# Performance work log

Hardware: AMD Instinct MI355X
Metric: run time of the kernel (lower is better)

The kernel has to match this reference:

```python
import jax, jax.numpy as jnp
import numpy as np

B, S, HID, NH, MAX_TOKENS = 2, 2048, 2048, 16, 2048
HD = HID // NH

def rotate_half(x):
    x1, x2 = x[..., :x.shape[-1] // 2], x[..., x.shape[-1] // 2:]
    return jnp.concatenate((-x2, x1), axis=-1)

def rope_tables():
    inv_freq = 1.0 / (10000.0 ** (jnp.arange(0, HD, 2, dtype=jnp.float32) / HD))
    t = jnp.arange(MAX_TOKENS, dtype=jnp.float32)
    freqs = jnp.outer(t, inv_freq)                       # [T, HD/2]
    emb = jnp.concatenate((freqs, freqs), axis=-1)       # [T, HD]
    return jnp.cos(emb), jnp.sin(emb)

def setup_inputs() -> dict:
    key = jax.random.key(0)
    ks = jax.random.split(key, 5)
    hidden_states = jax.random.normal(ks[0], (B, S, HID), dtype=jnp.float32)
    # additive causal mask [B, 1, S, S]: 0 on/below diag, large negative above
    neg = jnp.finfo(jnp.float32).min
    causal = jnp.where(jnp.tril(jnp.ones((S, S), dtype=bool)), 0.0, neg)
    attention_mask = jnp.broadcast_to(causal[None, None], (B, 1, S, S)).astype(jnp.float32)
    position_ids = jnp.broadcast_to(jnp.arange(S, dtype=jnp.int32), (B, S))
    scale = 1.0 / np.sqrt(HID)
    Wq = jax.random.normal(ks[1], (HID, HID), dtype=jnp.float32) * scale
    Wk = jax.random.normal(ks[2], (HID, HID), dtype=jnp.float32) * scale
    Wv = jax.random.normal(ks[3], (HID, HID), dtype=jnp.float32) * scale
    Wo = jax.random.normal(ks[4], (HID, HID), dtype=jnp.float32) * scale
    return {"hidden_states": hidden_states, "attention_mask": attention_mask,
            "position_ids": position_ids, "Wq": Wq, "Wk": Wk, "Wv": Wv, "Wo": Wo}

def reference(hidden_states, attention_mask, position_ids, Wq, Wk, Wv, Wo):
    b, s, _ = hidden_states.shape
    def proj(W):  # torch Linear: x @ W.T -> [b, H, s, hd]
        return (hidden_states @ W.T).reshape(b, s, NH, HD).transpose(0, 2, 1, 3)
    q, k, v = proj(Wq), proj(Wk), proj(Wv)
    cos_t, sin_t = rope_tables()
    cos = cos_t[position_ids][:, None]   # [b, 1, s, hd]
    sin = sin_t[position_ids][:, None]
    q = q * cos + rotate_half(q) * sin
    k = k * cos + rotate_half(k) * sin
    scores = jnp.einsum('bhqd,bhkd->bhqk', q, k) / np.sqrt(HD)
    scores = jnp.maximum(scores + attention_mask, jnp.finfo(scores.dtype).min)
    attn = jax.nn.softmax(scores.astype(jnp.float32), axis=-1).astype(q.dtype)
    out = jnp.einsum('bhqk,bhkd->bhqd', attn, v)
    out = out.transpose(0, 2, 1, 3).reshape(b, s, HID)
    return out @ Wo.T
```

## Files before the change

### kernel.cpp

```cpp
#include <hip/hip_runtime.h>

#define B_   2
#define S_   2048
#define HID_ 2048
#define NH_  16
#define HD_  128
#define MAXTOK_ 2048

typedef float  f32x4  __attribute__((ext_vector_type(4)));
typedef __bf16 bf16x8 __attribute__((ext_vector_type(8)));
typedef unsigned short u16x8 __attribute__((ext_vector_type(8)));

__device__ __forceinline__ unsigned short f2bf(float f) {
  union { float fv; unsigned u; } v; v.fv = f;
  unsigned r = v.u + 0x7FFFu + ((v.u >> 16) & 1u);
  return (unsigned short)(r >> 16);
}
__device__ __forceinline__ float bf2f(unsigned short h) {
  union { unsigned u; float fv; } v; v.u = ((unsigned)h) << 16;
  return v.fv;
}

__device__ __forceinline__ void gload16(const void* g, void* lds) {
  __builtin_amdgcn_global_load_lds(
      (const __attribute__((address_space(1))) void*)g,
      (__attribute__((address_space(3))) void*)lds, 16, 0, 0);
}

#define H4_ (B_ * S_ * HID_ / 4)
#define W4_ (HID_ * HID_ / 4)
__global__ void cast_all(const float* __restrict__ h,  const float* __restrict__ wq,
                         const float* __restrict__ wk, const float* __restrict__ wv,
                         const float* __restrict__ wo,
                         unsigned short* __restrict__ xb,  unsigned short* __restrict__ wqb,
                         unsigned short* __restrict__ wkb, unsigned short* __restrict__ wvb,
                         unsigned short* __restrict__ wob) {
  const int total = H4_ + 4 * W4_;
  int i = blockIdx.x * blockDim.x + threadIdx.x;
  int stride = gridDim.x * blockDim.x;
  for (; i < total; i += stride) {
    const float* src; unsigned short* dst; int j;
    if (i < H4_) { src = h; dst = xb; j = i; }
    else {
      int k = i - H4_, wsel = k >> 20;
      j = k & (W4_ - 1);
      src = (wsel == 0) ? wq : (wsel == 1) ? wk : (wsel == 2) ? wv : wo;
      dst = (wsel == 0) ? wqb : (wsel == 1) ? wkb : (wsel == 2) ? wvb : wob;
    }
    float4 v = ((const float4*)src)[j];
    ushort4 o;
    o.x = f2bf(v.x); o.y = f2bf(v.y); o.z = f2bf(v.z); o.w = f2bf(v.w);
    ((ushort4*)dst)[j] = o;
  }
}

#define QKV_STG(gp, lp, rb) gload16((gp) + (size_t)(rb) * 2048, (lp) + (rb) * 64)

#define QKV_LOADA(Q) do { \
  _Pragma("unroll") \
  for (int mi_ = 0; mi_ < 2; ++mi_) { \
    const char* rp_ = (const char*)Acur + (size_t)((wm + (Q) * 32 + mi_ * 16 + rowq) * 128); \
    af[mi_][0] = *(const bf16x8*)(rp_ + cb0); \
    af[mi_][1] = *(const bf16x8*)(rp_ + cb1); \
  } } while (0)

#define QKV_LOADB() do { \
  _Pragma("unroll") \
  for (int ni_ = 0; ni_ < 3; ++ni_) { \
    const char* rp_ = (const char*)Bcur + (size_t)((wn + ni_ * 16 + rowq) * 128); \
    bfr[ni_][0] = *(const bf16x8*)(rp_ + cb0); \
    bfr[ni_][1] = *(const bf16x8*)(rp_ + cb1); \
  } } while (0)

#define QKV_MFMA(Q) do { \
  _Pragma("unroll") \
  for (int mi_ = 0; mi_ < 2; ++mi_) { \
    _Pragma("unroll") \
    for (int ni_ = 0; ni_ < 3; ++ni_) { \
      f32x4 c_ = acc[(Q) * 2 + mi_][ni_]; \
      c_ = __builtin_amdgcn_mfma_f32_16x16x32_bf16(af[mi_][0], bfr[ni_][0], c_, 0, 0, 0); \
      c_ = __builtin_amdgcn_mfma_f32_16x16x32_bf16(af[mi_][1], bfr[ni_][1], c_, 0, 0, 0); \
      acc[(Q) * 2 + mi_][ni_] = c_; \
    } } } while (0)

#define QKV_BAR    asm volatile("s_barrier" ::: "memory")
#define QKV_VMC4   asm volatile("s_waitcnt vmcnt(4)" ::: "memory")
#define QKV_VMC2   asm volatile("s_waitcnt vmcnt(2)" ::: "memory")
#define QKV_VMC0   asm volatile("s_waitcnt vmcnt(0)" ::: "memory")

__global__ __launch_bounds__(512, 2)
void gemm_qkv(const unsigned short* __restrict__ A,
              const unsigned short* __restrict__ Bw,
              unsigned short* __restrict__ Qb,
              unsigned short* __restrict__ Kb,
              unsigned short* __restrict__ Vtmp) {
  const int K = HID_;
  const int NT = K / 64;
  __shared__ __align__(16) unsigned short As[2][256 * 64];
  __shared__ __align__(16) unsigned short Bs[2][192 * 64];

  const int tid = threadIdx.x, lane = tid & 63, w = tid >> 6;
  const int n0 = blockIdx.x * 192, m0 = blockIdx.y * 256;
  const int wm = (w >> 2) * 128, wn = (w & 3) * 48;
  const int rowq = lane & 15, klane = lane >> 4;
  const int sw  = (rowq & 7) << 4;
  const int cb0 = (klane * 16) ^ sw;
  const int cb1 = ((klane + 4) * 16) ^ sw;
  const int srow = tid >> 3;
  const int dc8  = (tid & 7) * 8;
  const int scol = (((tid & 7) * 16) ^ ((srow & 7) << 4)) >> 1;

  const unsigned short* Ag = A  + (size_t)(m0 + srow) * K + scol;
  const unsigned short* Bg = Bw + (size_t)(n0 + srow) * K + scol;

  f32x4 acc[8][3];
#pragma unroll
  for (int i = 0; i < 8; ++i)
#pragma unroll
    for (int j = 0; j < 3; ++j)
#pragma unroll
      for (int r = 0; r < 4; ++r) acc[i][j][r] = 0.f;

  bf16x8 af[2][2], bfr[3][2];

  {
    unsigned short* Al = (unsigned short*)&As[0][0] + srow * 64 + dc8;
    unsigned short* Bl = (unsigned short*)&Bs[0][0] + srow * 64 + dc8;
    QKV_STG(Bg, Bl, 0); QKV_STG(Bg, Bl, 64); QKV_STG(Bg, Bl, 128);
    QKV_STG(Ag, Al, 0); QKV_STG(Ag, Al, 128);
    QKV_STG(Ag, Al, 64); QKV_STG(Ag, Al, 192);
  }
  QKV_VMC2;
  QKV_BAR;

  const unsigned short* Acur = &As[0][0];
  const unsigned short* Bcur = &Bs[0][0];
  unsigned short* Anx = (unsigned short*)&As[1][0];
  unsigned short* Bnx = (unsigned short*)&Bs[1][0];

  for (int t = 0; t < NT - 1; ++t) {
    const int kn = (t + 1) * 64;
    const unsigned short* Agk = Ag + kn;
    const unsigned short* Bgk = Bg + kn;
    unsigned short* Al = Anx + srow * 64 + dc8;
    unsigned short* Bl = Bnx + srow * 64 + dc8;

    QKV_LOADA(0); QKV_LOADB();
    QKV_STG(Bgk, Bl, 0); QKV_STG(Bgk, Bl, 64);
    QKV_BAR;
    __builtin_amdgcn_s_setprio(1); QKV_MFMA(0); __builtin_amdgcn_s_setprio(0);
    QKV_BAR;
    QKV_LOADA(1);
    QKV_STG(Bgk, Bl, 128); QKV_STG(Agk, Al, 0);
    QKV_BAR;
    __builtin_amdgcn_s_setprio(1); QKV_MFMA(1); __builtin_amdgcn_s_setprio(0);
    QKV_VMC4;
    QKV_BAR;
    QKV_LOADA(2);
    QKV_STG(Agk, Al, 128); QKV_STG(Agk, Al, 64);
    QKV_BAR;
    __builtin_amdgcn_s_setprio(1); QKV_MFMA(2); __builtin_amdgcn_s_setprio(0);
    QKV_BAR;
    QKV_LOADA(3);
    QKV_STG(Agk, Al, 192);
    QKV_BAR;
    __builtin_amdgcn_s_setprio(1); QKV_MFMA(3); __builtin_amdgcn_s_setprio(0);
    QKV_VMC2;
    QKV_BAR;

    { const unsigned short* tp = Acur; Acur = Anx; Anx = (unsigned short*)tp; }
    { const unsigned short* tp = Bcur; Bcur = Bnx; Bnx = (unsigned short*)tp; }
  }

  QKV_LOADA(0); QKV_LOADB();
  QKV_BAR;
  __builtin_amdgcn_s_setprio(1); QKV_MFMA(0); __builtin_amdgcn_s_setprio(0);
  QKV_BAR;
  QKV_LOADA(1);
  QKV_BAR;
  __builtin_amdgcn_s_setprio(1); QKV_MFMA(1); __builtin_amdgcn_s_setprio(0);
  QKV_VMC0;
  QKV_BAR;
  QKV_LOADA(2);
  QKV_BAR;
  __builtin_amdgcn_s_setprio(1); QKV_MFMA(2); __builtin_amdgcn_s_setprio(0);
  QKV_BAR;
  QKV_LOADA(3);
  __builtin_amdgcn_s_setprio(1); QKV_MFMA(3); __builtin_amdgcn_s_setprio(0);

  const int lr0 = klane * 4;
#pragma unroll
  for (int mi = 0; mi < 8; ++mi)
#pragma unroll
    for (int ni = 0; ni < 3; ++ni)
#pragma unroll
      for (int r = 0; r < 4; ++r) {
        int r_ = m0 + wm + mi * 16 + lr0 + r;
        int c_ = n0 + wn + ni * 16 + rowq;
        float v = acc[mi][ni][r];
        int b = r_ >> 11, s = r_ & 2047;
        int proj = c_ >> 11, cin = c_ & 2047;
        if (proj == 2) {
          Vtmp[(size_t)(b * S_ + s) * HID_ + cin] = f2bf(v);
        } else {
          int hh = cin >> 7, d = cin & 127;
          unsigned short* dst = (proj == 0) ? Qb : Kb;
          dst[(((size_t)(b * NH_ + hh) * S_ + s) * HD_) + d] = f2bf(v);
        }
      }
}

#define OUT_LOADB() do { \
  _Pragma("unroll") \
  for (int ni_ = 0; ni_ < 2; ++ni_) { \
    const char* rp_ = (const char*)Bcur + (size_t)((wn + ni_ * 16 + rowq) * 128); \
    bfr[ni_][0] = *(const bf16x8*)(rp_ + cb0); \
    bfr[ni_][1] = *(const bf16x8*)(rp_ + cb1); \
  } } while (0)

#define OUT_MFMA(Q) do { \
  _Pragma("unroll") \
  for (int mi_ = 0; mi_ < 2; ++mi_) { \
    _Pragma("unroll") \
    for (int ni_ = 0; ni_ < 2; ++ni_) { \
      f32x4 c_ = acc[(Q) * 2 + mi_][ni_]; \
      c_ = __builtin_amdgcn_mfma_f32_16x16x32_bf16(af[mi_][0], bfr[ni_][0], c_, 0, 0, 0); \
      c_ = __builtin_amdgcn_mfma_f32_16x16x32_bf16(af[mi_][1], bfr[ni_][1], c_, 0, 0, 0); \
      acc[(Q) * 2 + mi_][ni_] = c_; \
    } } } while (0)

__global__ __launch_bounds__(512, 2)
void gemm_out(const unsigned short* __restrict__ A,
              const unsigned short* __restrict__ Bw,
              float* __restrict__ Cout) {
  const int K = HID_, N = HID_;
  const int NT = K / 64;
  __shared__ __align__(16) unsigned short As[2][256 * 64];
  __shared__ __align__(16) unsigned short Bs[2][128 * 64];

  const int tid = threadIdx.x, lane = tid & 63, w = tid >> 6;
  const int n0 = blockIdx.x * 128, m0 = blockIdx.y * 256;
  const int wm = (w >> 2) * 128, wn = (w & 3) * 32;
  const int rowq = lane & 15, klane = lane >> 4;
  const int sw  = (rowq & 7) << 4;
  const int cb0 = (klane * 16) ^ sw;
  const int cb1 = ((klane + 4) * 16) ^ sw;
  const int srow = tid >> 3;
  const int dc8  = (tid & 7) * 8;
  const int scol = (((tid & 7) * 16) ^ ((srow & 7) << 4)) >> 1;

  const unsigned short* Ag = A  + (size_t)(m0 + srow) * K + scol;
  const unsigned short* Bg = Bw + (size_t)(n0 + srow) * K + scol;

  f32x4 acc[8][2];
#pragma unroll
  for (int i = 0; i < 8; ++i)
#pragma unroll
    for (int j = 0; j < 2; ++j)
#pragma unroll
      for (int r = 0; r < 4; ++r) acc[i][j][r] = 0.f;

  bf16x8 af[2][2], bfr[2][2];

  {
    unsigned short* Al = (unsigned short*)&As[0][0] + srow * 64 + dc8;
    unsigned short* Bl = (unsigned short*)&Bs[0][0] + srow * 64 + dc8;
    QKV_STG(Bg, Bl, 0); QKV_STG(Bg, Bl, 64);
    QKV_STG(Ag, Al, 0); QKV_STG(Ag, Al, 128);
    QKV_STG(Ag, Al, 64); QKV_STG(Ag, Al, 192);
  }
  QKV_VMC2;
  QKV_BAR;

  const unsigned short* Acur = &As[0][0];
  const unsigned short* Bcur = &Bs[0][0];
  unsigned short* Anx = (unsigned short*)&As[1][0];
  unsigned short* Bnx = (unsigned short*)&Bs[1][0];

  for (int t = 0; t < NT - 1; ++t) {
    const int kn = (t + 1) * 64;
    const unsigned short* Agk = Ag + kn;
    const unsigned short* Bgk = Bg + kn;
    unsigned short* Al = Anx + srow * 64 + dc8;
    unsigned short* Bl = Bnx + srow * 64 + dc8;

    QKV_LOADA(0); OUT_LOADB();
    QKV_STG(Bgk, Bl, 0); QKV_STG(Bgk, Bl, 64);
    QKV_BAR;
    __builtin_amdgcn_s_setprio(1); OUT_MFMA(0); __builtin_amdgcn_s_setprio(0);
    QKV_BAR;
    QKV_LOADA(1);
    QKV_STG(Agk, Al, 0); QKV_STG(Agk, Al, 128);
    QKV_BAR;
    __builtin_amdgcn_s_setprio(1); OUT_MFMA(1); __builtin_amdgcn_s_setprio(0);
    QKV_VMC4;
    QKV_BAR;
    QKV_LOADA(2);
    QKV_STG(Agk, Al, 64);
    QKV_BAR;
    __builtin_amdgcn_s_setprio(1); OUT_MFMA(2); __builtin_amdgcn_s_setprio(0);
    QKV_BAR;
    QKV_LOADA(3);
    QKV_STG(Agk, Al, 192);
    QKV_BAR;
    __builtin_amdgcn_s_setprio(1); OUT_MFMA(3); __builtin_amdgcn_s_setprio(0);
    QKV_VMC2;
    QKV_BAR;

    { const unsigned short* tp = Acur; Acur = Anx; Anx = (unsigned short*)tp; }
    { const unsigned short* tp = Bcur; Bcur = Bnx; Bnx = (unsigned short*)tp; }
  }

  QKV_LOADA(0); OUT_LOADB();
  QKV_BAR;
  __builtin_amdgcn_s_setprio(1); OUT_MFMA(0); __builtin_amdgcn_s_setprio(0);
  QKV_BAR;
  QKV_LOADA(1);
  QKV_BAR;
  __builtin_amdgcn_s_setprio(1); OUT_MFMA(1); __builtin_amdgcn_s_setprio(0);
  QKV_VMC0;
  QKV_BAR;
  QKV_LOADA(2);
  QKV_BAR;
  __builtin_amdgcn_s_setprio(1); OUT_MFMA(2); __builtin_amdgcn_s_setprio(0);
  QKV_BAR;
  QKV_LOADA(3);
  __builtin_amdgcn_s_setprio(1); OUT_MFMA(3); __builtin_amdgcn_s_setprio(0);

  const int lr0 = klane * 4;
#pragma unroll
  for (int mi = 0; mi < 8; ++mi)
#pragma unroll
    for (int ni = 0; ni < 2; ++ni)
#pragma unroll
      for (int r = 0; r < 4; ++r) {
        int r_ = m0 + wm + mi * 16 + lr0 + r;
        int c_ = n0 + wn + ni * 16 + rowq;
        Cout[(size_t)r_ * N + c_] = acc[mi][ni][r];
      }
}

__global__ void rope_table(float2* __restrict__ tbl) {
  int i = blockIdx.x * blockDim.x + threadIdx.x;
  if (i >= MAXTOK_ * 64) return;
  int p = i >> 6, d = i & 63;
  float f = __expf(-(float)d * (9.210340371976184f / 64.f));
  float sn, cs;
  __sincosf((float)p * f, &sn, &cs);
  tbl[i] = make_float2(cs, sn);
}

#define QSCALE_ 0.12751744f
__global__ __launch_bounds__(256)
void rope_apply(unsigned short* __restrict__ Qb, unsigned short* __restrict__ Kb,
                const int* __restrict__ pos_ids, const float2* __restrict__ tbl) {
  int i = blockIdx.x * blockDim.x + threadIdx.x;
  int t8 = i & 7, bhs = i >> 3;
  int s = bhs & (S_ - 1);
  int b = bhs >> 15;
  int d0 = t8 * 8;
  int p = pos_ids[b * S_ + s];
  const float2* tp = tbl + p * 64 + d0;
  float cs[8], sn[8];
#pragma unroll
  for (int j = 0; j < 8; ++j) { float2 c2 = tp[j]; cs[j] = c2.x; sn[j] = c2.y; }
  size_t base = (size_t)bhs * HD_ + d0;
  {
    u16x8 x1 = *(const u16x8*)(Qb + base);
    u16x8 x2 = *(const u16x8*)(Qb + base + 64);
    u16x8 o1, o2;
#pragma unroll
    for (int j = 0; j < 8; ++j) {
      float a = bf2f(x1[j]), bb = bf2f(x2[j]);
      o1[j] = f2bf((a * cs[j] - bb * sn[j]) * QSCALE_);
      o2[j] = f2bf((bb * cs[j] + a * sn[j]) * QSCALE_);
    }
    *(u16x8*)(Qb + base) = o1;
    *(u16x8*)(Qb + base + 64) = o2;
  }
  {
    u16x8 x1 = *(const u16x8*)(Kb + base);
    u16x8 x2 = *(const u16x8*)(Kb + base + 64);
    u16x8 o1, o2;
#pragma unroll
    for (int j = 0; j < 8; ++j) {
      float a = bf2f(x1[j]), bb = bf2f(x2[j]);
      o1[j] = f2bf(a * cs[j] - bb * sn[j]);
      o2[j] = f2bf(bb * cs[j] + a * sn[j]);
    }
    *(u16x8*)(Kb + base) = o1;
    *(u16x8*)(Kb + base + 64) = o2;
  }
}

__global__ __launch_bounds__(256)
void transpose_v(const unsigned short* __restrict__ Vin,
                 unsigned short* __restrict__ Vt) {
  __shared__ __align__(16) unsigned short t[64 * 72];
  const int s0 = blockIdx.x * 64, d0 = blockIdx.y * 64, bh = blockIdx.z;
  const int b = bh >> 4, h = bh & 15;
  const int tid = threadIdx.x;
#pragma unroll
  for (int it = 0; it < 2; ++it) {
    int chunk = it * 256 + tid;
    int sl = chunk >> 3, dc = (chunk & 7) * 8;
    u16x8 v = *(const u16x8*)&Vin[(size_t)(b * S_ + s0 + sl) * HID_ + h * HD_ + d0 + dc];
    *(u16x8*)&t[sl * 72 + dc] = v;
  }
  __syncthreads();
#pragma unroll
  for (int it = 0; it < 2; ++it) {
    int lin = it * 256 + tid;
    int dl = lin & 63, sq = (lin >> 6) * 8;
    u16x8 v;
#pragma unroll
    for (int j = 0; j < 8; ++j) v[j] = t[(sq + j) * 72 + dl];
    *(u16x8*)&Vt[((size_t)bh * HD_ + d0 + dl) * S_ + s0 + sq] = v;
  }
}

#define KS_LD 136
#define VS_LD 72
#define PS_LD 72
__global__ __launch_bounds__(256, 2)
void attn_fused(const unsigned short* __restrict__ Qb,
                const unsigned short* __restrict__ Kb,
                const unsigned short* __restrict__ Vt,
                unsigned short* __restrict__ Ob) {
  __shared__ __align__(16) unsigned short Ks[64 * KS_LD];
  __shared__ __align__(16) unsigned short Vts[128 * VS_LD];
  __shared__ __align__(16) unsigned short Ps[4 * 16 * PS_LD];

  const int tid = threadIdx.x, lane = tid & 63, w = tid >> 6;
  const int bh = blockIdx.x;
  const int qt = (gridDim.y - 1) - blockIdx.y;
  const int q0 = qt * 64;
  const int b = bh >> 4, h = bh & 15;
  const int rowq = lane & 15;
  const int koff = (lane >> 4) * 8;
  const int lr0 = (lane >> 4) * 4;
  const size_t qkbase = (size_t)bh * (S_ * HD_);
  const size_t vbase  = (size_t)bh * (HD_ * S_);

  bf16x8 qf0, qf1, qf2, qf3;
  {
    const unsigned short* qrow = Qb + qkbase + (size_t)(q0 + w * 16 + rowq) * HD_;
    qf0 = *(const bf16x8*)(qrow + 0 * 32 + koff);
    qf1 = *(const bf16x8*)(qrow + 1 * 32 + koff);
    qf2 = *(const bf16x8*)(qrow + 2 * 32 + koff);
    qf3 = *(const bf16x8*)(qrow + 3 * 32 + koff);
  }

  const int krow = tid >> 4, kcol = (tid & 15) * 8;
  const int vrow = tid >> 3, vcol = (tid & 7) * 8;
  const unsigned short* kptr = Kb + qkbase + (size_t)krow * HD_ + kcol;
  const unsigned short* vptr = Vt + vbase + (size_t)vrow * S_ + vcol;

  f32x4 oacc[8];
  for (int i = 0; i < 8; ++i)
    for (int r = 0; r < 4; ++r) oacc[i][r] = 0.f;
  float m_r[4] = {-3e38f, -3e38f, -3e38f, -3e38f};
  float l_r[4] = {0.f, 0.f, 0.f, 0.f};

  const int nkt = qt + 1;

  float4 k0, k1, k2, k3, v0, v1, v2, v3;
  k0 = *(const float4*)(kptr + 0 * 16 * HD_);
  k1 = *(const float4*)(kptr + 1 * 16 * HD_);
  k2 = *(const float4*)(kptr + 2 * 16 * HD_);
  k3 = *(const float4*)(kptr + 3 * 16 * HD_);
  v0 = *(const float4*)(vptr + 0 * 32 * S_);
  v1 = *(const float4*)(vptr + 1 * 32 * S_);
  v2 = *(const float4*)(vptr + 2 * 32 * S_);
  v3 = *(const float4*)(vptr + 3 * 32 * S_);

  for (int kt = 0; kt < nkt; ++kt) {
    __syncthreads();
    *(float4*)&Ks[(krow + 0 * 16) * KS_LD + kcol] = k0;
    *(float4*)&Ks[(krow + 1 * 16) * KS_LD + kcol] = k1;
    *(float4*)&Ks[(krow + 2 * 16) * KS_LD + kcol] = k2;
    *(float4*)&Ks[(krow + 3 * 16) * KS_LD + kcol] = k3;
    *(float4*)&Vts[(vrow + 0 * 32) * VS_LD + vcol] = v0;
    *(float4*)&Vts[(vrow + 1 * 32) * VS_LD + vcol] = v1;
    *(float4*)&Vts[(vrow + 2 * 32) * VS_LD + vcol] = v2;
    *(float4*)&Vts[(vrow + 3 * 32) * VS_LD + vcol] = v3;
    if (kt + 1 < nkt) {
      const unsigned short* kp = kptr + (size_t)(kt + 1) * 64 * HD_;
      k0 = *(const float4*)(kp + 0 * 16 * HD_);
      k1 = *(const float4*)(kp + 1 * 16 * HD_);
      k2 = *(const float4*)(kp + 2 * 16 * HD_);
      k3 = *(const float4*)(kp + 3 * 16 * HD_);
    }
    __syncthreads();

    f32x4 sacc[4];
    for (int n = 0; n < 4; ++n)
      for (int r = 0; r < 4; ++r) sacc[n][r] = 0.f;
#pragma unroll
    for (int n = 0; n < 4; ++n) {
      const unsigned short* krow_p = &Ks[(n * 16 + rowq) * KS_LD + koff];
      sacc[n] = __builtin_amdgcn_mfma_f32_16x16x32_bf16(qf0, *(const bf16x8*)(krow_p + 0 * 32), sacc[n], 0, 0, 0);
      sacc[n] = __builtin_amdgcn_mfma_f32_16x16x32_bf16(qf1, *(const bf16x8*)(krow_p + 1 * 32), sacc[n], 0, 0, 0);
      sacc[n] = __builtin_amdgcn_mfma_f32_16x16x32_bf16(qf2, *(const bf16x8*)(krow_p + 2 * 32), sacc[n], 0, 0, 0);
      sacc[n] = __builtin_amdgcn_mfma_f32_16x16x32_bf16(qf3, *(const bf16x8*)(krow_p + 3 * 32), sacc[n], 0, 0, 0);
    }

    float tmax[4] = {-3e38f, -3e38f, -3e38f, -3e38f};
    if (kt == qt) {
      for (int n = 0; n < 4; ++n) {
        int col = n * 16 + rowq;
        for (int r = 0; r < 4; ++r) {
          int row = w * 16 + lr0 + r;
          float x = (col <= row) ? sacc[n][r] : -1e30f;
          sacc[n][r] = x;
          tmax[r] = fmaxf(tmax[r], x);
        }
      }
    } else {
      for (int n = 0; n < 4; ++n)
        for (int r = 0; r < 4; ++r)
          tmax[r] = fmaxf(tmax[r], sacc[n][r]);
    }
    for (int off = 1; off < 16; off <<= 1)
      for (int r = 0; r < 4; ++r) tmax[r] = fmaxf(tmax[r], __shfl_xor(tmax[r], off));
    float alpha[4];
    for (int r = 0; r < 4; ++r) {
      float mn = fmaxf(m_r[r], tmax[r]);
      alpha[r] = __builtin_amdgcn_exp2f(m_r[r] - mn);
      m_r[r] = mn;
    }
    float rs[4] = {0.f, 0.f, 0.f, 0.f};
    for (int n = 0; n < 4; ++n)
      for (int r = 0; r < 4; ++r) {
        float p = __builtin_amdgcn_exp2f(sacc[n][r] - m_r[r]);
        sacc[n][r] = p;
        rs[r] += p;
      }
    for (int off = 1; off < 16; off <<= 1)
      for (int r = 0; r < 4; ++r) rs[r] += __shfl_xor(rs[r], off);
    for (int r = 0; r < 4; ++r) l_r[r] = l_r[r] * alpha[r] + rs[r];
    for (int nd = 0; nd < 8; ++nd)
      for (int r = 0; r < 4; ++r) oacc[nd][r] *= alpha[r];

    if (kt + 1 < nkt) {
      const unsigned short* vp = vptr + (size_t)(kt + 1) * 64;
      v0 = *(const float4*)(vp + 0 * 32 * S_);
      v1 = *(const float4*)(vp + 1 * 32 * S_);
      v2 = *(const float4*)(vp + 2 * 32 * S_);
      v3 = *(const float4*)(vp + 3 * 32 * S_);
    }

    unsigned short* pw = &Ps[w * 16 * PS_LD];
    for (int n = 0; n < 4; ++n)
      for (int r = 0; r < 4; ++r)
        pw[(lr0 + r) * PS_LD + n * 16 + rowq] = f2bf(sacc[n][r]);

#pragma unroll
    for (int t2 = 0; t2 < 2; ++t2) {
      bf16x8 pa = *(const bf16x8*)&pw[rowq * PS_LD + t2 * 32 + koff];
      for (int nd = 0; nd < 8; ++nd) {
        bf16x8 vb = *(const bf16x8*)&Vts[(nd * 16 + rowq) * VS_LD + t2 * 32 + koff];
        oacc[nd] = __builtin_amdgcn_mfma_f32_16x16x32_bf16(pa, vb, oacc[nd], 0, 0, 0);
      }
    }
  }

  float linv[4];
  for (int r = 0; r < 4; ++r) linv[r] = __builtin_amdgcn_rcpf(l_r[r]);
  for (int nd = 0; nd < 8; ++nd) {
    int col = h * HD_ + nd * 16 + rowq;
    for (int r = 0; r < 4; ++r) {
      int row = q0 + w * 16 + lr0 + r;
      Ob[(size_t)(b * S_ + row) * HID_ + col] = f2bf(oacc[nd][r] * linv[r]);
    }
  }
}

extern "C" void kernel_launch(void* const* d_in, const int* in_sizes, int n_in,
                              void* d_out, int out_size, void* d_ws, size_t ws_size,
                              hipStream_t stream) {
  (void)in_sizes; (void)n_in; (void)out_size; (void)ws_size;
  const float* hidden = (const float*)d_in[0];
  const int* pos = (const int*)d_in[2];
  const float* Wq = (const float*)d_in[3];
  const float* Wk = (const float*)d_in[4];
  const float* Wv = (const float*)d_in[5];
  const float* Wo = (const float*)d_in[6];
  float* out = (float*)d_out;

  char* ws = (char*)d_ws;
  unsigned short* Xb   = (unsigned short*)(ws);
  unsigned short* Wqb  = (unsigned short*)(ws + 16777216);
  unsigned short* Wkb  = (unsigned short*)(ws + 25165824);
  unsigned short* Wvb  = (unsigned short*)(ws + 33554432);
  unsigned short* Wob  = (unsigned short*)(ws + 41943040);
  unsigned short* Qb   = (unsigned short*)(ws + 50331648);
  unsigned short* Kb   = (unsigned short*)(ws + 67108864);
  unsigned short* Vtmp = (unsigned short*)(ws + 83886080);
  unsigned short* Vtb  = (unsigned short*)(ws + 100663296);
  unsigned short* Ob   = Xb;
  float2* tbl          = (float2*)ws;

  cast_all<<<2048, 256, 0, stream>>>(hidden, Wq, Wk, Wv, Wo, Xb, Wqb, Wkb, Wvb, Wob);

  dim3 gq(3 * HID_ / 192, (B_ * S_) / 256);
  gemm_qkv<<<gq, 512, 0, stream>>>(Xb, Wqb, Qb, Kb, Vtmp);

  rope_table<<<(MAXTOK_ * 64) / 256, 256, 0, stream>>>(tbl);
  rope_apply<<<(B_ * NH_ * S_ * 8) / 256, 256, 0, stream>>>(Qb, Kb, pos, tbl);

  dim3 tg(S_ / 64, HD_ / 64, B_ * NH_);
  transpose_v<<<tg, 256, 0, stream>>>(Vtmp, Vtb);

  dim3 ag(B_ * NH_, S_ / 64);
  attn_fused<<<ag, 256, 0, stream>>>(Qb, Kb, Vtb, Ob);

  dim3 go(HID_ / 128, (B_ * S_) / 256);
  gemm_out<<<go, 512, 0, stream>>>(Ob, Wob, out);
}
```

Baseline: 407.9 us.

## Restructure attention with 128-row query tiles, async LDS loads and swizzled K/V

The attention kernel now processes 128 query rows per 512-thread block. K is double-buffered and K and V tiles are staged with direct global-to-LDS loads into XOR-swizzled layouts. Query tiles are reordered so that long and short causal blocks interleave, and explicit vmcnt waits overlap K/V loading with the MFMA work. This targets the register round-trip and the padded LDS stores of the old staging, and improves load balance. The cost is more LDS per block and occupancy limits from the new launch bounds. The out-projection GEMM also gets its own A-fragment load macro, apparently fixing a macro reuse.

```diff
diff --git a/kernel.cpp b/kernel.cpp
--- a/kernel.cpp
+++ b/kernel.cpp
@@ -210,6 +210,14 @@
       }
 }
 
+#define OUT_LOADA(Q) do { \
+  _Pragma("unroll") \
+  for (int mi_ = 0; mi_ < 2; ++mi_) { \
+    const char* rp_ = (const char*)Acur + (size_t)((wm + (Q) * 32 + mi_ * 16 + rowq) * 128); \
+    af[mi_][0] = *(const bf16x8*)(rp_ + cb0); \
+    af[mi_][1] = *(const bf16x8*)(rp_ + cb1); \
+  } } while (0)
+
 #define OUT_LOADB() do { \
   _Pragma("unroll") \
   for (int ni_ = 0; ni_ < 2; ++ni_) { \
@@ -284,23 +292,23 @@
     unsigned short* Al = Anx + srow * 64 + dc8;
     unsigned short* Bl = Bnx + srow * 64 + dc8;
 
-    QKV_LOADA(0); OUT_LOADB();
+    OUT_LOADA(0); OUT_LOADB();
     QKV_STG(Bgk, Bl, 0); QKV_STG(Bgk, Bl, 64);
     QKV_BAR;
     __builtin_amdgcn_s_setprio(1); OUT_MFMA(0); __builtin_amdgcn_s_setprio(0);
     QKV_BAR;
-    QKV_LOADA(1);
+    OUT_LOADA(1);
     QKV_STG(Agk, Al, 0); QKV_STG(Agk, Al, 128);
     QKV_BAR;
     __builtin_amdgcn_s_setprio(1); OUT_MFMA(1); __builtin_amdgcn_s_setprio(0);
     QKV_VMC4;
     QKV_BAR;
-    QKV_LOADA(2);
+    OUT_LOADA(2);
     QKV_STG(Agk, Al, 64);
     QKV_BAR;
     __builtin_amdgcn_s_setprio(1); OUT_MFMA(2); __builtin_amdgcn_s_setprio(0);
     QKV_BAR;
-    QKV_LOADA(3);
+    OUT_LOADA(3);
     QKV_STG(Agk, Al, 192);
     QKV_BAR;
     __builtin_amdgcn_s_setprio(1); OUT_MFMA(3); __builtin_amdgcn_s_setprio(0);
@@ -311,20 +319,20 @@
     { const unsigned short* tp = Bcur; Bcur = Bnx; Bnx = (unsigned short*)tp; }
   }
 
-  QKV_LOADA(0); OUT_LOADB();
+  OUT_LOADA(0); OUT_LOADB();
   QKV_BAR;
   __builtin_amdgcn_s_setprio(1); OUT_MFMA(0); __builtin_amdgcn_s_setprio(0);
   QKV_BAR;
-  QKV_LOADA(1);
+  OUT_LOADA(1);
   QKV_BAR;
   __builtin_amdgcn_s_setprio(1); OUT_MFMA(1); __builtin_amdgcn_s_setprio(0);
   QKV_VMC0;
   QKV_BAR;
-  QKV_LOADA(2);
+  OUT_LOADA(2);
   QKV_BAR;
   __builtin_amdgcn_s_setprio(1); OUT_MFMA(2); __builtin_amdgcn_s_setprio(0);
   QKV_BAR;
-  QKV_LOADA(3);
+  OUT_LOADA(3);
   __builtin_amdgcn_s_setprio(1); OUT_MFMA(3); __builtin_amdgcn_s_setprio(0);
 
   const int lr0 = klane * 4;
@@ -419,28 +427,32 @@
   }
 }
 
-#define KS_LD 136
-#define VS_LD 72
 #define PS_LD 72
-__global__ __launch_bounds__(256, 2)
+__global__ __launch_bounds__(512, 4)
 void attn_fused(const unsigned short* __restrict__ Qb,
                 const unsigned short* __restrict__ Kb,
                 const unsigned short* __restrict__ Vt,
                 unsigned short* __restrict__ Ob) {
-  __shared__ __align__(16) unsigned short Ks[64 * KS_LD];
-  __shared__ __align__(16) unsigned short Vts[128 * VS_LD];
-  __shared__ __align__(16) unsigned short Ps[4 * 16 * PS_LD];
+  __shared__ __align__(16) unsigned short Ks[2][64 * 128];
+  __shared__ __align__(16) unsigned short Vts[128 * 64];
+  __shared__ __align__(16) unsigned short Ps[8 * 16 * PS_LD];
 
   const int tid = threadIdx.x, lane = tid & 63, w = tid >> 6;
   const int bh = blockIdx.x;
-  const int qt = (gridDim.y - 1) - blockIdx.y;
-  const int q0 = qt * 64;
+  const int qtb = blockIdx.y;
+  const int qtv = (qtb < 8) ? (15 - qtb) : (qtb - 8);
+  const int q0 = qtv * 128;
   const int b = bh >> 4, h = bh & 15;
-  const int rowq = lane & 15;
-  const int koff = (lane >> 4) * 8;
-  const int lr0 = (lane >> 4) * 4;
+  const int rowq = lane & 15, klane = lane >> 4;
+  const int koff = klane * 8;
+  const int lr0 = klane * 4;
   const size_t qkbase = (size_t)bh * (S_ * HD_);
   const size_t vbase  = (size_t)bh * (HD_ * S_);
+
+  int cbK0 = ((0 * 4 + klane) ^ (rowq & 7)) << 4;
+  int cbK1 = ((1 * 4 + klane) ^ (rowq & 7)) << 4;
+  int cbK2 = ((2 * 4 + klane) ^ (rowq & 7)) << 4;
+  int cbK3 = ((3 * 4 + klane) ^ (rowq & 7)) << 4;
 
   bf16x8 qf0, qf1, qf2, qf3;
   {
@@ -451,124 +463,150 @@
     qf3 = *(const bf16x8*)(qrow + 3 * 32 + koff);
   }
 
-  const int krow = tid >> 4, kcol = (tid & 15) * 8;
-  const int vrow = tid >> 3, vcol = (tid & 7) * 8;
-  const unsigned short* kptr = Kb + qkbase + (size_t)krow * HD_ + kcol;
-  const unsigned short* vptr = Vt + vbase + (size_t)vrow * S_ + vcol;
+  const int krl = tid >> 4;
+  const int ksl = tid & 15;
+  const int scolK = ((ksl ^ (krl & 7)) * 8);
+  const unsigned short* Kg = Kb + qkbase + (size_t)krl * HD_ + scolK;
+  unsigned short* Kdst = (unsigned short*)Ks + krl * 128 + ksl * 8;
+  const int vrl = tid >> 3;
+  const int vsl = tid & 7;
+  const int scolV = ((vsl ^ (vrl & 7)) * 8);
+  const unsigned short* Vg = Vt + vbase + (size_t)vrl * S_ + scolV;
+  unsigned short* Vdst = (unsigned short*)Vts + vrl * 64 + vsl * 8;
+
+#define ATT_STAGE_K(KT, BUF) do { \
+  gload16(Kg + (size_t)((KT) * 64) * HD_,      Kdst + (BUF) * (64 * 128)); \
+  gload16(Kg + (size_t)((KT) * 64 + 32) * HD_, Kdst + (BUF) * (64 * 128) + 32 * 128); \
+} while (0)
+#define ATT_STAGE_V(KT) do { \
+  gload16(Vg + (KT) * 64,                   Vdst); \
+  gload16(Vg + (size_t)64 * S_ + (KT) * 64, Vdst + 64 * 64); \
+} while (0)
 
   f32x4 oacc[8];
+#pragma unroll
   for (int i = 0; i < 8; ++i)
+#pragma unroll
     for (int r = 0; r < 4; ++r) oacc[i][r] = 0.f;
   float m_r[4] = {-3e38f, -3e38f, -3e38f, -3e38f};
   float l_r[4] = {0.f, 0.f, 0.f, 0.f};
 
-  const int nkt = qt + 1;
-
-  float4 k0, k1, k2, k3, v0, v1, v2, v3;
-  k0 = *(const float4*)(kptr + 0 * 16 * HD_);
-  k1 = *(const float4*)(kptr + 1 * 16 * HD_);
-  k2 = *(const float4*)(kptr + 2 * 16 * HD_);
-  k3 = *(const float4*)(kptr + 3 * 16 * HD_);
-  v0 = *(const float4*)(vptr + 0 * 32 * S_);
-  v1 = *(const float4*)(vptr + 1 * 32 * S_);
-  v2 = *(const float4*)(vptr + 2 * 32 * S_);
-  v3 = *(const float4*)(vptr + 3 * 32 * S_);
+  const int nkt = 2 * qtv + 2;
+  int cur = 0;
+
+  ATT_STAGE_K(0, 0);
 
   for (int kt = 0; kt < nkt; ++kt) {
     __syncthreads();
-    *(float4*)&Ks[(krow + 0 * 16) * KS_LD + kcol] = k0;
-    *(float4*)&Ks[(krow + 1 * 16) * KS_LD + kcol] = k1;
-    *(float4*)&Ks[(krow + 2 * 16) * KS_LD + kcol] = k2;
-    *(float4*)&Ks[(krow + 3 * 16) * KS_LD + kcol] = k3;
-    *(float4*)&Vts[(vrow + 0 * 32) * VS_LD + vcol] = v0;
-    *(float4*)&Vts[(vrow + 1 * 32) * VS_LD + vcol] = v1;
-    *(float4*)&Vts[(vrow + 2 * 32) * VS_LD + vcol] = v2;
-    *(float4*)&Vts[(vrow + 3 * 32) * VS_LD + vcol] = v3;
-    if (kt + 1 < nkt) {
-      const unsigned short* kp = kptr + (size_t)(kt + 1) * 64 * HD_;
-      k0 = *(const float4*)(kp + 0 * 16 * HD_);
-      k1 = *(const float4*)(kp + 1 * 16 * HD_);
-      k2 = *(const float4*)(kp + 2 * 16 * HD_);
-      k3 = *(const float4*)(kp + 3 * 16 * HD_);
+    ATT_STAGE_V(kt);
+    const bool hn = (kt + 1 < nkt);
+    if (hn) {
+      ATT_STAGE_K(kt + 1, cur ^ 1);
+      asm volatile("s_waitcnt vmcnt(4)" ::: "memory");
+    } else {
+      asm volatile("s_waitcnt vmcnt(2)" ::: "memory");
     }
     __syncthreads();
 
+    const unsigned short* Kc = (const unsigned short*)Ks + cur * (64 * 128);
     f32x4 sacc[4];
+#pragma unroll
     for (int n = 0; n < 4; ++n)
+#pragma unroll
       for (int r = 0; r < 4; ++r) sacc[n][r] = 0.f;
 #pragma unroll
     for (int n = 0; n < 4; ++n) {
-      const unsigned short* krow_p = &Ks[(n * 16 + rowq) * KS_LD + koff];
-      sacc[n] = __builtin_amdgcn_mfma_f32_16x16x32_bf16(qf0, *(const bf16x8*)(krow_p + 0 * 32), sacc[n], 0, 0, 0);
-      sacc[n] = __builtin_amdgcn_mfma_f32_16x16x32_bf16(qf1, *(const bf16x8*)(krow_p + 1 * 32), sacc[n], 0, 0, 0);
-      sacc[n] = __builtin_amdgcn_mfma_f32_16x16x32_bf16(qf2, *(const bf16x8*)(krow_p + 2 * 32), sacc[n], 0, 0, 0);
-      sacc[n] = __builtin_amdgcn_mfma_f32_16x16x32_bf16(qf3, *(const bf16x8*)(krow_p + 3 * 32), sacc[n], 0, 0, 0);
+      const char* rp = (const char*)(Kc + (n * 16 + rowq) * 128);
+      sacc[n] = __builtin_amdgcn_mfma_f32_16x16x32_bf16(qf0, *(const bf16x8*)(rp + cbK0), sacc[n], 0, 0, 0);
+      sacc[n] = __builtin_amdgcn_mfma_f32_16x16x32_bf16(qf1, *(const bf16x8*)(rp + cbK1), sacc[n], 0, 0, 0);
+      sacc[n] = __builtin_amdgcn_mfma_f32_16x16x32_bf16(qf2, *(const bf16x8*)(rp + cbK2), sacc[n], 0, 0, 0);
+      sacc[n] = __builtin_amdgcn_mfma_f32_16x16x32_bf16(qf3, *(const bf16x8*)(rp + cbK3), sacc[n], 0, 0, 0);
     }
 
     float tmax[4] = {-3e38f, -3e38f, -3e38f, -3e38f};
-    if (kt == qt) {
+    if (kt >= 2 * qtv) {
+      const int cbase = (kt - 2 * qtv) * 64;
+#pragma unroll
       for (int n = 0; n < 4; ++n) {
-        int col = n * 16 + rowq;
+        int coll = cbase + n * 16 + rowq;
+#pragma unroll
         for (int r = 0; r < 4; ++r) {
-          int row = w * 16 + lr0 + r;
-          float x = (col <= row) ? sacc[n][r] : -1e30f;
+          int rowl = w * 16 + lr0 + r;
+          float x = (coll <= rowl) ? sacc[n][r] : -1e30f;
           sacc[n][r] = x;
           tmax[r] = fmaxf(tmax[r], x);
         }
       }
     } else {
+#pragma unroll
       for (int n = 0; n < 4; ++n)
+#pragma unroll
         for (int r = 0; r < 4; ++r)
           tmax[r] = fmaxf(tmax[r], sacc[n][r]);
     }
+#pragma unroll
     for (int off = 1; off < 16; off <<= 1)
+#pragma unroll
       for (int r = 0; r < 4; ++r) tmax[r] = fmaxf(tmax[r], __shfl_xor(tmax[r], off));
     float alpha[4];
+#pragma unroll
     for (int r = 0; r < 4; ++r) {
       float mn = fmaxf(m_r[r], tmax[r]);
       alpha[r] = __builtin_amdgcn_exp2f(m_r[r] - mn);
       m_r[r] = mn;
     }
     float rs[4] = {0.f, 0.f, 0.f, 0.f};
+#pragma unroll
     for (int n = 0; n < 4; ++n)
+#pragma unroll
       for (int r = 0; r < 4; ++r) {
         float p = __builtin_amdgcn_exp2f(sacc[n][r] - m_r[r]);
         sacc[n][r] = p;
         rs[r] += p;
       }
+#pragma unroll
     for (int off = 1; off < 16; off <<= 1)
+#pragma unroll
       for (int r = 0; r < 4; ++r) rs[r] += __shfl_xor(rs[r], off);
+#pragma unroll
     for (int r = 0; r < 4; ++r) l_r[r] = l_r[r] * alpha[r] + rs[r];
+#pragma unroll
     for (int nd = 0; nd < 8; ++nd)
+#pragma unroll
       for (int r = 0; r < 4; ++r) oacc[nd][r] *= alpha[r];
 
-    if (kt + 1 < nkt) {
-      const unsigned short* vp = vptr + (size_t)(kt + 1) * 64;
-      v0 = *(const float4*)(vp + 0 * 32 * S_);
-      v1 = *(const float4*)(vp + 1 * 32 * S_);
-      v2 = *(const float4*)(vp + 2 * 32 * S_);
-      v3 = *(const float4*)(vp + 3 * 32 * S_);
-    }
+    if (hn) { asm volatile("s_waitcnt vmcnt(2)" ::: "memory"); }
+    else    { asm volatile("s_waitcnt vmcnt(0)" ::: "memory"); }
+    __syncthreads();
 
     unsigned short* pw = &Ps[w * 16 * PS_LD];
+#pragma unroll
     for (int n = 0; n < 4; ++n)
+#pragma unroll
       for (int r = 0; r < 4; ++r)
         pw[(lr0 + r) * PS_LD + n * 16 + rowq] = f2bf(sacc[n][r]);
 
 #pragma unroll
     for (int t2 = 0; t2 < 2; ++t2) {
       bf16x8 pa = *(const bf16x8*)&pw[rowq * PS_LD + t2 * 32 + koff];
+      const int cbv = ((t2 * 4 + klane) ^ (rowq & 7)) << 4;
+#pragma unroll
       for (int nd = 0; nd < 8; ++nd) {
-        bf16x8 vb = *(const bf16x8*)&Vts[(nd * 16 + rowq) * VS_LD + t2 * 32 + koff];
+        const char* vp = (const char*)((const unsigned short*)Vts + (nd * 16 + rowq) * 64);
+        bf16x8 vb = *(const bf16x8*)(vp + cbv);
         oacc[nd] = __builtin_amdgcn_mfma_f32_16x16x32_bf16(pa, vb, oacc[nd], 0, 0, 0);
       }
     }
+    cur ^= 1;
   }
 
   float linv[4];
+#pragma unroll
   for (int r = 0; r < 4; ++r) linv[r] = __builtin_amdgcn_rcpf(l_r[r]);
+#pragma unroll
   for (int nd = 0; nd < 8; ++nd) {
     int col = h * HD_ + nd * 16 + rowq;
+#pragma unroll
     for (int r = 0; r < 4; ++r) {
       int row = q0 + w * 16 + lr0 + r;
       Ob[(size_t)(b * S_ + row) * HID_ + col] = f2bf(oacc[nd][r] * linv[r]);
@@ -612,8 +650,8 @@
   dim3 tg(S_ / 64, HD_ / 64, B_ * NH_);
   transpose_v<<<tg, 256, 0, stream>>>(Vtmp, Vtb);
 
-  dim3 ag(B_ * NH_, S_ / 64);
-  attn_fused<<<ag, 256, 0, stream>>>(Qb, Kb, Vtb, Ob);
+  dim3 ag(B_ * NH_, S_ / 128);
+  attn_fused<<<ag, 512, 0, stream>>>(Qb, Kb, Vtb, Ob);
 
   dim3 go(HID_ / 128, (B_ * S_) / 256);
   gemm_out<<<go, 512, 0, stream>>>(Ob, Wob, out);
```

Result: no change. 414.0 us (+1.5%).
